# Optimization experiments

Measured on AMD Instinct MI355X. Metric: run time of the kernel, lower is better.

The kernel has to match this reference:

```python
import jax, jax.numpy as jnp
import numpy as np

DIM = 64
SQRT_DIM = np.sqrt(DIM).astype(np.float32)
NEG_INF = -1e9


def setup_inputs() -> dict:
    key = jax.random.key(0)
    kq, kk, kv, km = jax.random.split(key, 4)
    B, Q, K, D = 32, 1024, 1024, DIM
    query = jax.random.normal(kq, (B, Q, D), dtype=jnp.float32)
    k = jax.random.normal(kk, (B, K, D), dtype=jnp.float32)
    value = jax.random.normal(kv, (B, K, D), dtype=jnp.float32)
    mask = jax.random.randint(km, (B, Q, K), 0, 2).astype(jnp.bool_)
    return {"query": query, "key": k, "value": value, "mask": mask}


def reference(query, key, value, mask):
    # score: [B, Q, K]
    score = jnp.einsum('bqd,bkd->bqk', query, key) / SQRT_DIM
    score = jnp.where(mask, NEG_INF, score)
    attn = jax.nn.softmax(score, axis=-1)
    context = jnp.einsum('bqk,bkd->bqd', attn, value)
    return (context, attn)
```

## Files before the change

kernel.cpp:

```cpp
#include <hip/hip_runtime.h>

constexpr int BATCH = 32;
constexpr int QLEN  = 1024;
constexpr int KLEN  = 1024;
constexpr int DIM   = 64;
constexpr int TQ    = 16;

typedef float    f32x4 __attribute__((ext_vector_type(4)));
typedef int      i32x4 __attribute__((ext_vector_type(4)));
typedef _Float16 f16x8 __attribute__((ext_vector_type(8)));
typedef _Float16 f16x4 __attribute__((ext_vector_type(4)));
typedef unsigned long long u64;
typedef unsigned int u32;

__device__ __forceinline__ f16x8 cvt_h8(f32x4 a, f32x4 b) {
  f16x8 h;
  h[0] = (_Float16)a[0]; h[1] = (_Float16)a[1]; h[2] = (_Float16)a[2]; h[3] = (_Float16)a[3];
  h[4] = (_Float16)b[0]; h[5] = (_Float16)b[1]; h[6] = (_Float16)b[2]; h[7] = (_Float16)b[3];
  return h;
}

constexpr int TK = 128;
__global__ __launch_bounds__(256)
void vtkh_kernel(const float* __restrict__ V, const float* __restrict__ Kg,
                 _Float16* __restrict__ Vt, _Float16* __restrict__ Kh) {
  __shared__ _Float16 lt[DIM][TK + 8];
  const int b = blockIdx.y, k0 = blockIdx.x * TK;
  const int t = threadIdx.x;
  const int d4 = (t & 15) * 4;
  #pragma unroll
  for (int p = 0; p < TK / 16; ++p) {
    const int kl = (t >> 4) + p * 16;
    const f32x4 v = *(const f32x4*)(V + ((size_t)(b * KLEN + k0 + kl)) * DIM + d4);
    #pragma unroll
    for (int j = 0; j < 4; ++j) lt[d4 + j][kl] = (_Float16)v[j];
  }
  #pragma unroll
  for (int p = 0; p < 8; ++p) {
    const int idx = t + p * 256;
    const int kl = idx >> 4, dd = (idx & 15) * 4;
    const f32x4 v = *(const f32x4*)(Kg + ((size_t)(b * KLEN + k0 + kl)) * DIM + dd);
    f16x4 h = { (_Float16)v[0], (_Float16)v[1], (_Float16)v[2], (_Float16)v[3] };
    *(f16x4*)(Kh + ((size_t)(b * KLEN + k0 + kl)) * DIM + dd) = h;
  }
  __syncthreads();
  const int d = t >> 2;
  #pragma unroll
  for (int j2 = 0; j2 < TK / 32; ++j2) {
    const int seg = (t & 3) + j2 * 4;
    *(f16x8*)(Vt + (size_t)b * DIM * KLEN + (size_t)d * KLEN + k0 + seg * 8) =
        *(const f16x8*)(&lt[d][seg * 8]);
  }
}

__global__ __launch_bounds__(256, 4)
void sdpa_kernel(const float* __restrict__ Qg, const _Float16* __restrict__ Kh,
                 const _Float16* __restrict__ Vt, const int* __restrict__ Mg,
                 float* __restrict__ Ctx, float* __restrict__ Attn)
{
  __shared__ float rs[4][16];
  __shared__ __attribute__((aligned(16))) _Float16 sp[TQ * 1024];

  const int tid  = threadIdx.x;
  const int w    = tid >> 6;
  const int l    = tid & 63;
  const int n16  = l & 15;
  const int quad = l >> 4;
  char* const spb = (char*)sp;

  const int lin = blockIdx.x;
  const int b   = lin >> 6;
  const int q0  = (lin & 63) * TQ;

  const float qscl = 0.125f * 1.44269504f;
  const float* qb = Qg + ((size_t)(b * QLEN + q0 + n16)) * DIM + quad * 8;
  f32x4 qa0 = *(const f32x4*)(qb),      qa1 = *(const f32x4*)(qb + 4);
  f32x4 qa2 = *(const f32x4*)(qb + 32), qa3 = *(const f32x4*)(qb + 36);
  #pragma unroll
  for (int i = 0; i < 4; ++i) { qa0[i] *= qscl; qa1[i] *= qscl; qa2[i] *= qscl; qa3[i] *= qscl; }
  const f16x8 aq0 = cvt_h8(qa0, qa1);
  const f16x8 aq1 = cvt_h8(qa2, qa3);

  const _Float16* kb = Kh + (size_t)b * KLEN * DIM + quad * 8;
  const int* mrow = Mg + ((size_t)(b * QLEN + q0 + n16)) * KLEN + w * 256 + quad * 4;

  f32x4 rsum4 = {0.f, 0.f, 0.f, 0.f};
  f16x4 ec[16];
  #pragma unroll
  for (int tt = 0; tt < 16; ++tt) {
    const i32x4 mv = *(const i32x4*)(mrow + tt * 16);
    const _Float16* kp = kb + (size_t)((w * 16 + tt) * 16 + n16) * DIM;
    const f16x8 ak0 = *(const f16x8*)(kp);
    const f16x8 ak1 = *(const f16x8*)(kp + 32);
    f32x4 acc = {0.f, 0.f, 0.f, 0.f};
    acc = __builtin_amdgcn_mfma_f32_16x16x32_f16(ak0, aq0, acc, 0, 0, 0);
    acc = __builtin_amdgcn_mfma_f32_16x16x32_f16(ak1, aq1, acc, 0, 0, 0);
    f32x4 e;
    #pragma unroll
    for (int i = 0; i < 4; ++i) {
      e[i] = mv[i] ? 0.f : __builtin_amdgcn_exp2f(acc[i]);
      rsum4[i] += e[i];
    }
    ec[tt] = f16x4{ (_Float16)e[0], (_Float16)e[1], (_Float16)e[2], (_Float16)e[3] };
  }
  float rsum = (rsum4[0] + rsum4[1]) + (rsum4[2] + rsum4[3]);
  rsum += __shfl_xor(rsum, 16, 64);
  rsum += __shfl_xor(rsum, 32, 64);
  if (quad == 0) rs[w][n16] = rsum;
  __syncthreads();
  const float inv =
      __builtin_amdgcn_rcpf(rs[0][n16] + rs[1][n16] + rs[2][n16] + rs[3][n16]);

  #pragma unroll
  for (int tt = 0; tt < 16; ++tt) {
    f32x4 ev;
    #pragma unroll
    for (int i = 0; i < 4; ++i) ev[i] = (float)ec[tt][i] * inv;
    f16x4 ph = { (_Float16)ev[0], (_Float16)ev[1], (_Float16)ev[2], (_Float16)ev[3] };
    const int g = w * 64 + tt * 4 + quad;
    *(f16x4*)(spb + (n16 << 11) + ((g * 8) ^ ((n16 & 7) << 4))) = ph;
  }
  __syncthreads();

  #pragma unroll
  for (int rr = 0; rr < 4; ++rr) {
    const int row = w * 4 + rr;
    float* arow = Attn + ((size_t)(b * QLEN + q0 + row)) * KLEN;
    #pragma unroll
    for (int j = 0; j < 4; ++j) {
      const int g = j * 64 + l;
      const f16x4 hv = *(const f16x4*)(spb + (row << 11) + ((g * 8) ^ ((row & 7) << 4)));
      f32x4 ov = { (float)hv[0], (float)hv[1], (float)hv[2], (float)hv[3] };
      *(f32x4*)(arow + j * 256 + l * 4) = ov;
    }
  }

  const _Float16* vtb = Vt + ((size_t)(b * DIM + w * 16 + n16)) * KLEN;
  f32x4 c0 = {0.f, 0.f, 0.f, 0.f}, c1 = {0.f, 0.f, 0.f, 0.f};
  #pragma unroll 8
  for (int m = 0; m < 32; m += 2) {
    const int ga = m * 8 + quad * 2;
    const f16x8 pa0 = *(const f16x8*)(spb + (n16 << 11) + ((ga * 8) ^ ((n16 & 7) << 4)));
    const f16x8 pa1 = *(const f16x8*)(spb + (n16 << 11) + (((ga + 8) * 8) ^ ((n16 & 7) << 4)));
    const f16x8 bv0 = *(const f16x8*)(vtb + m * 32 + quad * 8);
    const f16x8 bv1 = *(const f16x8*)(vtb + (m + 1) * 32 + quad * 8);
    c0 = __builtin_amdgcn_mfma_f32_16x16x32_f16(bv0, pa0, c0, 0, 0, 0);
    c1 = __builtin_amdgcn_mfma_f32_16x16x32_f16(bv1, pa1, c1, 0, 0, 0);
  }
  f32x4 cv = { c0[0] + c1[0], c0[1] + c1[1], c0[2] + c1[2], c0[3] + c1[3] };
  *(f32x4*)(Ctx + ((size_t)(b * QLEN + q0 + n16)) * DIM + w * 16 + quad * 4) = cv;
}

extern "C" void kernel_launch(void* const* d_in, const int* in_sizes, int n_in,
                              void* d_out, int out_size, void* d_ws, size_t ws_size,
                              hipStream_t stream) {
  const float* Qg = (const float*)d_in[0];
  const float* Kg = (const float*)d_in[1];
  const float* Vg = (const float*)d_in[2];
  const int*   Mg = (const int*)d_in[3];
  float* Ctx  = (float*)d_out;
  float* Attn = (float*)d_out + (size_t)BATCH * QLEN * DIM;
  _Float16* Vt = (_Float16*)d_ws;
  _Float16* Kh = (_Float16*)((char*)d_ws + (size_t)BATCH * DIM * KLEN * 2);

  dim3 tgrid(KLEN / TK, BATCH);
  vtkh_kernel<<<tgrid, 256, 0, stream>>>(Vg, Kg, Vt, Kh);

  sdpa_kernel<<<2048, 256, 0, stream>>>(Qg, Kh, Vt, Mg, Ctx, Attn);
}
```

Measured before the change: 305.5 us.

## Defer softmax normalization to output stores and prefetch mask with nontemporal loads

Unnormalized fp16 exponentials are now written straight to shared memory during the score loop. The reciprocal row sum is applied when writing attention rows and when writing the context accumulator. This removes the register-held ec array, a second normalization pass and one block barrier. All 16 mask vectors are also loaded up front with nontemporal hints to overlap the mask fetch with the QK compute. The cost is higher register pressure from mv[16], and the PV matmul now runs on unnormalized fp16 values.

Measured after the change: 309.5 us. No clear change (+1.3%).

```diff
diff --git a/kernel.cpp b/kernel.cpp
--- a/kernel.cpp
+++ b/kernel.cpp
@@ -72,6 +72,13 @@
   const int b   = lin >> 6;
   const int q0  = (lin & 63) * TQ;
 
+  const int* mrow = Mg + ((size_t)(b * QLEN + q0 + n16)) * KLEN + w * 256 + quad * 4;
+
+  i32x4 mv[16];
+  #pragma unroll
+  for (int tt = 0; tt < 16; ++tt)
+    mv[tt] = __builtin_nontemporal_load((const i32x4*)(mrow + tt * 16));
+
   const float qscl = 0.125f * 1.44269504f;
   const float* qb = Qg + ((size_t)(b * QLEN + q0 + n16)) * DIM + quad * 8;
   f32x4 qa0 = *(const f32x4*)(qb),      qa1 = *(const f32x4*)(qb + 4);
@@ -82,55 +89,44 @@
   const f16x8 aq1 = cvt_h8(qa2, qa3);
 
   const _Float16* kb = Kh + (size_t)b * KLEN * DIM + quad * 8;
-  const int* mrow = Mg + ((size_t)(b * QLEN + q0 + n16)) * KLEN + w * 256 + quad * 4;
 
   f32x4 rsum4 = {0.f, 0.f, 0.f, 0.f};
-  f16x4 ec[16];
   #pragma unroll
   for (int tt = 0; tt < 16; ++tt) {
-    const i32x4 mv = *(const i32x4*)(mrow + tt * 16);
     const _Float16* kp = kb + (size_t)((w * 16 + tt) * 16 + n16) * DIM;
     const f16x8 ak0 = *(const f16x8*)(kp);
     const f16x8 ak1 = *(const f16x8*)(kp + 32);
     f32x4 acc = {0.f, 0.f, 0.f, 0.f};
     acc = __builtin_amdgcn_mfma_f32_16x16x32_f16(ak0, aq0, acc, 0, 0, 0);
     acc = __builtin_amdgcn_mfma_f32_16x16x32_f16(ak1, aq1, acc, 0, 0, 0);
-    f32x4 e;
+    f16x4 ph;
     #pragma unroll
     for (int i = 0; i < 4; ++i) {
-      e[i] = mv[i] ? 0.f : __builtin_amdgcn_exp2f(acc[i]);
-      rsum4[i] += e[i];
+      const float e = mv[tt][i] ? 0.f : __builtin_amdgcn_exp2f(acc[i]);
+      rsum4[i] += e;
+      ph[i] = (_Float16)e;
     }
-    ec[tt] = f16x4{ (_Float16)e[0], (_Float16)e[1], (_Float16)e[2], (_Float16)e[3] };
+    const int g = w * 64 + tt * 4 + quad;
+    *(f16x4*)(spb + (n16 << 11) + ((g * 8) ^ ((n16 & 7) << 4))) = ph;
   }
   float rsum = (rsum4[0] + rsum4[1]) + (rsum4[2] + rsum4[3]);
   rsum += __shfl_xor(rsum, 16, 64);
   rsum += __shfl_xor(rsum, 32, 64);
   if (quad == 0) rs[w][n16] = rsum;
   __syncthreads();
-  const float inv =
-      __builtin_amdgcn_rcpf(rs[0][n16] + rs[1][n16] + rs[2][n16] + rs[3][n16]);
-
-  #pragma unroll
-  for (int tt = 0; tt < 16; ++tt) {
-    f32x4 ev;
-    #pragma unroll
-    for (int i = 0; i < 4; ++i) ev[i] = (float)ec[tt][i] * inv;
-    f16x4 ph = { (_Float16)ev[0], (_Float16)ev[1], (_Float16)ev[2], (_Float16)ev[3] };
-    const int g = w * 64 + tt * 4 + quad;
-    *(f16x4*)(spb + (n16 << 11) + ((g * 8) ^ ((n16 & 7) << 4))) = ph;
-  }
-  __syncthreads();
 
   #pragma unroll
   for (int rr = 0; rr < 4; ++rr) {
     const int row = w * 4 + rr;
+    const float invr =
+        __builtin_amdgcn_rcpf(rs[0][row] + rs[1][row] + rs[2][row] + rs[3][row]);
     float* arow = Attn + ((size_t)(b * QLEN + q0 + row)) * KLEN;
     #pragma unroll
     for (int j = 0; j < 4; ++j) {
       const int g = j * 64 + l;
       const f16x4 hv = *(const f16x4*)(spb + (row << 11) + ((g * 8) ^ ((row & 7) << 4)));
-      f32x4 ov = { (float)hv[0], (float)hv[1], (float)hv[2], (float)hv[3] };
+      f32x4 ov = { (float)hv[0] * invr, (float)hv[1] * invr,
+                   (float)hv[2] * invr, (float)hv[3] * invr };
       *(f32x4*)(arow + j * 256 + l * 4) = ov;
     }
   }
@@ -147,7 +143,10 @@
     c0 = __builtin_amdgcn_mfma_f32_16x16x32_f16(bv0, pa0, c0, 0, 0, 0);
     c1 = __builtin_amdgcn_mfma_f32_16x16x32_f16(bv1, pa1, c1, 0, 0, 0);
   }
-  f32x4 cv = { c0[0] + c1[0], c0[1] + c1[1], c0[2] + c1[2], c0[3] + c1[3] };
+  const float invq =
+      __builtin_amdgcn_rcpf(rs[0][n16] + rs[1][n16] + rs[2][n16] + rs[3][n16]);
+  f32x4 cv = { (c0[0] + c1[0]) * invq, (c0[1] + c1[1]) * invq,
+               (c0[2] + c1[2]) * invq, (c0[3] + c1[3]) * invq };
   *(f32x4*)(Ctx + ((size_t)(b * QLEN + q0 + n16)) * DIM + w * 16 + quad * 4) = cv;
 }
 
```
